# Kernel optimization log

Hardware: AMD Instinct MI355X
Metric: run time of the kernel (lower is better)

## Reference

```python
import jax, jax.numpy as jnp
import numpy as np

B, T, WN = 256, 200, 200        # batch, char_num, word_num
H, CD, WD = 512, 30, 128        # hidden_dim, char_dim, word_dim
V, K = 128, 12                  # vocab, tag_size
START, STOP = 10, 11
HH = H // 2


def lstm_dir(x_tm, m_tm, Wih, Whh, b, reverse):
    # x_tm: [T,B,I], m_tm: [T,B,1] validity mask. Packed-sequence semantics:
    # state only updates on valid steps, padded outputs are zero. reverse=True
    # replicates the backward direction of a packed bidirectional LSTM.
    z = jnp.zeros((x_tm.shape[1], Whh.shape[1]), x_tm.dtype)
    def cell(carry, inp):
        h, c = carry
        xt, mt = inp
        g = xt @ Wih.T + h @ Whh.T + b              # [B,4H], gates i,f,g,o
        i, f, gc, o = jnp.split(g, 4, axis=-1)
        cn = jax.nn.sigmoid(f) * c + jax.nn.sigmoid(i) * jnp.tanh(gc)
        hn = jax.nn.sigmoid(o) * jnp.tanh(cn)
        return (jnp.where(mt, hn, h), jnp.where(mt, cn, c)), jnp.where(mt, hn, 0.0)
    _, ys = jax.lax.scan(cell, (z, z), (x_tm, m_tm), reverse=reverse)
    return ys


def bilstm(x, lens, Wih_f, Whh_f, b_f, Wih_b, Whh_b, b_b):
    Tn = x.shape[1]
    m = jnp.arange(Tn)[None, :] < lens[:, None]     # [B,T]
    x_tm = jnp.swapaxes(x, 0, 1)
    m_tm = m.T[:, :, None]
    hf = lstm_dir(x_tm, m_tm, Wih_f, Whh_f, b_f, False)
    hb = lstm_dir(x_tm, m_tm, Wih_b, Whh_b, b_b, True)
    return jnp.swapaxes(jnp.concatenate([hf, hb], -1), 0, 1)  # [B,T,H]


def encode(characters, words, len_char, len_word,
           char_emb, char_Wih_f, char_Whh_f, char_b_f, char_Wih_b, char_Whh_b, char_b_b,
           char_lin_W, char_lin_b,
           word_Wih_f, word_Whh_f, word_b_f, word_Wih_b, word_Whh_b, word_b_b,
           word_lin_W, word_lin_b, lin1_W, lin1_b, lin2_W, lin2_b, tag_W, tag_b):
    sp = jax.nn.softplus
    char_vec = char_emb[characters]                                   # [B,T,CD]
    char_h = bilstm(char_vec, len_char, char_Wih_f, char_Whh_f, char_b_f,
                    char_Wih_b, char_Whh_b, char_b_b)                 # [B,T,H]
    char_map = sp(char_h @ char_lin_W.T + char_lin_b)                 # [B,T,H]
    word_h = bilstm(words, len_word, word_Wih_f, word_Whh_f, word_b_f,
                    word_Wih_b, word_Whh_b, word_b_b)                 # [B,WN,H]
    word_map = sp(word_h @ word_lin_W.T + word_lin_b)                 # [B,WN,T]
    word_map = word_map.reshape(word_map.shape[0], T, -1)             # view, NOT transpose
    x = jnp.concatenate([char_map, word_map], axis=2)                 # [B,T,712]
    x = sp(x @ lin1_W.T + lin1_b)
    x = sp(x @ lin2_W.T + lin2_b)
    return sp(x @ tag_W.T + tag_b)                                    # [B,T,K]


def crf_nll(logits, tags, lens, trans):
    Bn, Tn, Kn = logits.shape
    mask = jnp.arange(Tn)[None, :] < lens[:, None]                    # [B,T]
    # --- real path score (transitions indexed [from, to], START prepended) ---
    prev = jnp.concatenate([jnp.full((Bn, 1), START, tags.dtype), tags[:, :-1]], axis=1)
    emit = jnp.take_along_axis(logits, tags[..., None], axis=-1)[..., 0]
    step = jnp.where(mask, emit + trans[prev, tags], 0.0)
    last_tag = jnp.take_along_axis(tags, (lens - 1)[:, None], axis=1)[:, 0]
    real = step.sum(axis=1) + trans[last_tag, STOP]
    # --- forward algorithm (alpha init 0, first step includes transitions, as in source) ---
    def fwd(alpha, inp):
        lt, m = inp                                                   # [B,K], [B]
        sc = alpha[:, :, None] + lt[:, None, :] + trans[None]         # [B,prev,next]
        an = jax.nn.logsumexp(sc, axis=1)
        return jnp.where(m[:, None], an, alpha), None
    alpha0 = jnp.zeros((Bn, Kn), logits.dtype)
    alpha, _ = jax.lax.scan(fwd, alpha0, (jnp.swapaxes(logits, 0, 1), mask.T))
    total = jax.nn.logsumexp(alpha + trans[:, STOP][None, :], axis=1)
    return (jnp.sum(total) - jnp.sum(real)).reshape(1)


def setup_inputs() -> dict:
    key = jax.random.key(0)
    ks = jax.random.split(key, 32)
    rn = lambda k, s: jax.random.normal(k, s, jnp.float32) * 0.1
    inp = {
        "characters": jax.random.randint(ks[0], (B, T), 0, V),
        "words": jax.random.normal(ks[1], (B, WN, WD), jnp.float32),
        "tags": jax.random.randint(ks[2], (B, T), 0, K - 2),
        "len_char": jax.random.randint(ks[3], (B,), 50, T + 1),
        "len_word": jax.random.randint(ks[4], (B,), 50, WN + 1),
        "char_emb": rn(ks[5], (V, CD)),
        "char_Wih_f": rn(ks[6], (4 * HH, CD)), "char_Whh_f": rn(ks[7], (4 * HH, HH)), "char_b_f": rn(ks[8], (4 * HH,)),
        "char_Wih_b": rn(ks[9], (4 * HH, CD)), "char_Whh_b": rn(ks[10], (4 * HH, HH)), "char_b_b": rn(ks[11], (4 * HH,)),
        "char_lin_W": rn(ks[12], (H, H)), "char_lin_b": rn(ks[13], (H,)),
        "word_Wih_f": rn(ks[14], (4 * HH, WD)), "word_Whh_f": rn(ks[15], (4 * HH, HH)), "word_b_f": rn(ks[16], (4 * HH,)),
        "word_Wih_b": rn(ks[17], (4 * HH, WD)), "word_Whh_b": rn(ks[18], (4 * HH, HH)), "word_b_b": rn(ks[19], (4 * HH,)),
        "word_lin_W": rn(ks[20], (T, H)), "word_lin_b": rn(ks[21], (T,)),
        "lin1_W": rn(ks[22], (512, H + WN)), "lin1_b": rn(ks[23], (512,)),
        "lin2_W": rn(ks[24], (256, 512)), "lin2_b": rn(ks[25], (256,)),
        "tag_W": rn(ks[26], (K, 256)), "tag_b": rn(ks[27], (K,)),
    }
    trans = jax.random.normal(ks[28], (K, K), jnp.float32)
    trans = trans.at[START, :].set(-10000.0).at[:, STOP].set(-10000.0)
    inp["transitions"] = trans
    return inp


def reference(characters, words, tags, len_char, len_word,
              char_emb, char_Wih_f, char_Whh_f, char_b_f, char_Wih_b, char_Whh_b, char_b_b,
              char_lin_W, char_lin_b,
              word_Wih_f, word_Whh_f, word_b_f, word_Wih_b, word_Whh_b, word_b_b,
              word_lin_W, word_lin_b, lin1_W, lin1_b, lin2_W, lin2_b, tag_W, tag_b, transitions):
    logits = encode(characters, words, len_char, len_word,
                    char_emb, char_Wih_f, char_Whh_f, char_b_f, char_Wih_b, char_Whh_b, char_b_b,
                    char_lin_W, char_lin_b,
                    word_Wih_f, word_Whh_f, word_b_f, word_Wih_b, word_Whh_b, word_b_b,
                    word_lin_W, word_lin_b, lin1_W, lin1_b, lin2_W, lin2_b, tag_W, tag_b)
    return crf_nll(logits, tags, len_char, transitions)
```

## Files before the change

### kernel.cpp

```cpp
#include <hip/hip_runtime.h>
#include <cstdint>

typedef __attribute__((ext_vector_type(8))) short short8;
typedef __attribute__((ext_vector_type(4))) float f32x4;
typedef __attribute__((ext_vector_type(2))) float f32x2;
typedef __attribute__((ext_vector_type(4))) int i32x4;
typedef unsigned short us16;
typedef unsigned char u8;

#define DEV __device__ __forceinline__

DEV u8 f2fp8(float f){
  int p = __builtin_amdgcn_cvt_pk_fp8_f32(f, f, 0, false);
  return (u8)(p & 0xFF);
}
template<int SEL> DEV float fp8tof(int dw){
#if __has_builtin(__builtin_amdgcn_cvt_f32_fp8)
  return __builtin_amdgcn_cvt_f32_fp8(dw, SEL);
#else
  int b = (dw >> (8*SEL)) & 255;
  int e = (b>>3)&15, m = b&7;
  float v;
  if (e){ union{unsigned u; float f;} x; x.u = (unsigned)(((e+120)<<23) | (m<<20)); v = x.f; }
  else v = (float)m * 0.001953125f;
  return (b & 128) ? -v : v;
#endif
}
DEV f32x4 dq8x4(int dw){
#if __has_builtin(__builtin_amdgcn_cvt_pk_f32_fp8)
  f32x2 lo = __builtin_amdgcn_cvt_pk_f32_fp8(dw, false);
  f32x2 hi = __builtin_amdgcn_cvt_pk_f32_fp8(dw, true);
  return (f32x4){lo.x, lo.y, hi.x, hi.y};
#else
  return (f32x4){fp8tof<0>(dw), fp8tof<1>(dw), fp8tof<2>(dw), fp8tof<3>(dw)};
#endif
}
DEV float fsig(float x){
  float e = __builtin_amdgcn_exp2f(-1.4426950408889634f * x);
  return __builtin_amdgcn_rcpf(1.0f + e);
}
DEV float ftanh(float x){
  float e = __builtin_amdgcn_exp2f(-2.8853900817779268f * x);
  return fmaf(2.0f, __builtin_amdgcn_rcpf(1.0f + e), -1.0f);
}
DEV float fsoftplus(float x){
  float ax = fabsf(x);
  float e = __builtin_amdgcn_exp2f(-1.4426950408889634f * ax);
  float l = 0.69314718055994531f * __builtin_amdgcn_logf(1.0f + e);
  return fmaxf(x, 0.0f) + l;
}
DEV f32x4 mfma16f8(long a, long b, f32x4 c){
  return __builtin_amdgcn_mfma_f32_16x16x32_fp8_fp8(a, b, c, 0, 0, 0);
}
DEV unsigned pk4fp8(float a, float b, float c, float d){
  unsigned lo = (unsigned)__builtin_amdgcn_cvt_pk_fp8_f32(a, b, 0, false) & 0xFFFFu;
  unsigned hi = (unsigned)__builtin_amdgcn_cvt_pk_fp8_f32(c, d, 0, false) & 0xFFFFu;
  return lo | (hi << 16);
}

DEV void lds_barrier(){
  asm volatile("s_waitcnt lgkmcnt(0)" ::: "memory");
  __builtin_amdgcn_s_barrier();
  asm volatile("" ::: "memory");
}



DEV void swz_lstm16_one(int tid, const float* __restrict__ W, u8* __restrict__ dst){
  int e = tid & 511, chunk = tid >> 9;
  int L = e >> 3, j = e & 7;
  int kc = chunk & 7, gt = (chunk >> 3) & 3, w = chunk >> 5;
  int g = gt * 256 + w * 16 + (L & 15);
  int k = kc * 32 + (L >> 4) * 8 + j;
  dst[tid] = f2fp8(W[g * 256 + k]);
}

DEV void ctab_one(int vd, int gcol, const float* __restrict__ emb,
                  const float* __restrict__ Wih, const float* __restrict__ bb,
                  u8* __restrict__ ctab){
  int v = vd & 127, dir = vd >> 7;
  float val[4];
  #pragma unroll
  for (int gt = 0; gt < 4; ++gt){
    int g = gt * 256 + gcol;
    float s = bb[g];
    for (int k = 0; k < 30; ++k) s += emb[v * 30 + k] * Wih[g * 30 + k];
    val[gt] = s;
  }
  unsigned pk = pk4fp8(val[0], val[1], val[2], val[3]);
  *(unsigned*)&ctab[((dir * 128 + v) * 256 + gcol) * 4] = pk;
}

DEV void swz_gin_one(int tid, const float* __restrict__ W, u8* __restrict__ dst){
  int e = tid & 511, chunk = tid >> 9;
  int L = e >> 3, j = e & 7;
  int kc = chunk & 3, ntile = chunk >> 2;
  int g = ntile * 16 + (L & 15);
  int k = kc * 32 + (L >> 4) * 8 + j;
  dst[tid] = f2fp8(W[g * 128 + k]);
}

DEV void swz_ffB_one(int tid, const float* W, int N, int Kd, int KCs, u8* dst){
  int e = tid & 511, chunk = tid >> 9;
  int L = e >> 3, j = e & 7;
  int kc = chunk % KCs; int nt = chunk / KCs;
  int g = nt * 16 + (L & 15);
  int k = kc * 32 + (L >> 4) * 8 + j;
  float v = (g < N && k < Kd) ? W[g * Kd + k] : 0.0f;
  dst[tid] = f2fp8(v);
}

DEV void swz_ffA_one(int tid, const float* W, int Kd, int KCs, u8* dst){
  int e = tid & 511, chunk = tid >> 9;
  int L = e >> 3, j = e & 7;
  int kc = chunk % KCs; int mt = chunk / KCs;
  int m = mt * 16 + (L & 15);
  int k = kc * 32 + (L >> 4) * 8 + j;
  float v = (k < Kd) ? W[m * Kd + k] : 0.0f;
  dst[tid] = f2fp8(v);
}

__global__ __launch_bounds__(256) void k_pre(
    const float* __restrict__ words, u8* __restrict__ words_f8,
    const float* __restrict__ WhhA, u8* dA, const float* __restrict__ WhhB, u8* dB,
    const float* __restrict__ WhhC, u8* dC, const float* __restrict__ WhhD, u8* dD,
    const float* __restrict__ emb,
    const float* __restrict__ cWihF, const float* __restrict__ cbF,
    const float* __restrict__ cWihB, const float* __restrict__ cbB,
    u8* __restrict__ ctab,
    const float* __restrict__ gWf, const float* __restrict__ gWb,
    u8* __restrict__ dgf, u8* __restrict__ dgb,
    const float* __restrict__ W1, u8* d1, const float* __restrict__ W2, u8* d2,
    const float* __restrict__ W5, u8* d5,
    const float* __restrict__ W3, u8* d3, const float* __restrict__ W4, u8* d4)
{
  const int b = blockIdx.x, tid = threadIdx.x;
  if (b < 6400){
    int i = b * 256 + tid;
    f32x4 v = ((const f32x4*)words)[i];
    ((unsigned*)words_f8)[i] = pk4fp8(v.x, v.y, v.z, v.w);
  } else if (b < 10496){
    int bb = b - 6400;
    if (bb < 1024)       swz_lstm16_one(bb * 256 + tid, WhhA, dA);
    else if (bb < 2048)  swz_lstm16_one((bb - 1024) * 256 + tid, WhhB, dB);
    else if (bb < 3072)  swz_lstm16_one((bb - 2048) * 256 + tid, WhhC, dC);
    else                 swz_lstm16_one((bb - 3072) * 256 + tid, WhhD, dD);
  } else if (b < 10752){
    int vd = b - 10496;
    ctab_one(vd, tid, emb, (vd >> 7) ? cWihB : cWihF, (vd >> 7) ? cbB : cbF, ctab);
  } else if (b < 11776){
    int bb = b - 10752;
    if (bb < 512) swz_gin_one(bb * 256 + tid, gWf, dgf);
    else          swz_gin_one((bb - 512) * 256 + tid, gWb, dgb);
  } else if (b < 13328){
    int bb = b - 11776;
    if (bb < 1024)      swz_ffB_one(bb * 256 + tid, W1, 512, 512, 16, d1);
    else if (bb < 1536) swz_ffB_one((bb - 1024) * 256 + tid, W2, 200, 512, 16, d2);
    else                swz_ffB_one((bb - 1536) * 256 + tid, W5, 12, 256, 8, d5);
  } else {
    int bb = b - 13328;
    if (bb < 1536) swz_ffA_one(bb * 256 + tid, W3, 712, 24, d3);
    else           swz_ffA_one((bb - 1536) * 256 + tid, W4, 512, 16, d4);
  }
}

__global__ __launch_bounds__(512) void k_gin(
    const u8* __restrict__ words_f8, const u8* __restrict__ wswg_f,
    const u8* __restrict__ wswg_b, const float* __restrict__ bias_f,
    const float* __restrict__ bias_b, u8* __restrict__ gin)
{
  const int blk = blockIdx.x;
  const int d = blk / 800, rem = blk - d * 800;
  const int slice = rem / 50, tq = rem - slice * 50;
  const u8* Wsw = d ? wswg_b : wswg_f;
  const float* bias = d ? bias_b : bias_f;
  __shared__ u8 xs[16 * 136];
  __shared__ u8 sbuf[4 * 4096];
  const int tid = threadIdx.x;
  const int wv = tid >> 6, L = tid & 63;
  const int lrow = L & 15, lq = L >> 4;
  const long* WswV = (const long*)Wsw;

  long wr[8][4];
  #pragma unroll
  for (int nt = 0; nt < 8; ++nt)
    #pragma unroll
    for (int kc = 0; kc < 4; ++kc)
      wr[nt][kc] = WswV[((wv * 8 + nt) * 4 + kc) * 64 + L];
  float bv[8];
  #pragma unroll
  for (int nt = 0; nt < 8; ++nt) bv[nt] = bias[wv * 128 + nt * 16 + lrow];

  for (int i = 0; i < 4; ++i){
    const int t = tq * 4 + i;
    if (tid < 256){
      int r = tid >> 4, c8 = (tid & 15) * 8;
      *(long*)&xs[r * 136 + c8] =
        *(const long*)&words_f8[((long)(slice * 16 + r) * 200 + t) * 128 + c8];
    }
    __syncthreads();
    f32x4 acc[8];
    #pragma unroll
    for (int nt = 0; nt < 8; ++nt) acc[nt] = (f32x4){bv[nt], bv[nt], bv[nt], bv[nt]};
    #pragma unroll
    for (int kc = 0; kc < 4; ++kc){
      long af = *(const long*)&xs[lrow * 136 + kc * 32 + lq * 8];
      #pragma unroll
      for (int nt = 0; nt < 8; ++nt)
        acc[nt] = mfma16f8(af, wr[nt][kc], acc[nt]);
    }
    #pragma unroll
    for (int nt = 0; nt < 8; ++nt){
      int c = wv * 128 + nt * 16 + lrow;
      int gt = c >> 8, hcol = c & 255;
      int base = (hcol >> 4) * 256 + (hcol & 15) * 4 + gt;
      #pragma unroll
      for (int r = 0; r < 4; ++r)
        sbuf[lq * 4096 + base + r * 64] = f2fp8(acc[nt][r]);
    }
    __syncthreads();
    #pragma unroll
    for (int q = 0; q < 4; ++q){
      long ob = ((long)((d * 64 + slice * 4 + q) * 200 + t)) * 4096 + tid * 8;
      *(long*)&gin[ob] = *(const long*)&sbuf[q * 4096 + tid * 8];
    }
    __syncthreads();
  }
}

template<bool CHARV>
DEV void lstm16_body(u8* abuf, u8* cidxs,
                     const u8* __restrict__ gsrc,
                     const int* __restrict__ chars,
                     const u8* __restrict__ Wsw,
                     const int* __restrict__ lens,
                     u8* __restrict__ hout,
                     int b0, int hcol0, bool rev, long ginBase)
{
  const int tid = threadIdx.x;
  const int w = tid >> 6, L = tid & 63;
  const int lrow = L & 15, lq = L >> 4;
  const int gcol = w * 16 + lrow;
  const long* WswV = (const long*)Wsw;

  long wr[4][8];
  #pragma unroll
  for (int gt = 0; gt < 4; ++gt)
    #pragma unroll
    for (int kc = 0; kc < 8; ++kc)
      wr[gt][kc] = WswV[(((w * 4 + gt) * 8) + kc) * 64 + L];

  const int mylen = lens[b0 + lq];
  const long hbase = (long)(b0 + lq) * 200 * 512 + hcol0 + gcol;

  float cst = 0.0f;
  u8 hst = 0, houtv = 0;

  for (int e = tid; e < 1120; e += 1024) ((long*)abuf)[e] = 0;

  if constexpr (CHARV){
    if (tid < 800) cidxs[tid] = (u8)chars[(b0 + tid / 200) * 200 + tid % 200];
  }
  __syncthreads();

  const int t0 = rev ? 199 : 0;
  unsigned gw;
  if constexpr (!CHARV)
    gw = *(const unsigned*)(gsrc + (ginBase + t0) * 4096 + tid * 4);
  else
    gw = *(const unsigned*)&gsrc[((int)cidxs[lq * 200 + t0] * 256 + gcol) * 4];

  for (int tau = 0; tau < 200; ++tau){
    const int t = rev ? (199 - tau) : tau;
    u8* cur = abuf + (tau & 1) * 4480;
    u8* nxt = abuf + ((tau & 1) ^ 1) * 4480;

    f32x4 q = dq8x4((int)gw);
    f32x4 acc[4];
    #pragma unroll
    for (int gt = 0; gt < 4; ++gt)
      acc[gt] = (f32x4){q[gt], q[gt], q[gt], q[gt]};

    {
      const int tn = (tau < 199) ? (rev ? t - 1 : t + 1) : t;
      if constexpr (!CHARV)
        gw = *(const unsigned*)(gsrc + (ginBase + tn) * 4096 + tid * 4);
      else
        gw = *(const unsigned*)&gsrc[((int)cidxs[lq * 200 + tn] * 256 + gcol) * 4];
    }

    #pragma unroll
    for (int kc = 0; kc < 8; ++kc){
      long af = *(const long*)&cur[lrow * 280 + kc * 32 + lq * 8];
      #pragma unroll
      for (int gt = 0; gt < 4; ++gt)
        acc[gt] = mfma16f8(af, wr[gt][kc], acc[gt]);
    }

    const bool mk = t < mylen;
    float gi = acc[0][0], gf = acc[1][0];
    float gg = acc[2][0], go = acc[3][0];
    float cn = fsig(gf) * cst + fsig(gi) * ftanh(gg);
    if (mk) cst = cn;
    float hn = fsig(go) * ftanh(cn);
    u8 p8 = f2fp8(hn);
    if (mk) hst = p8;
    houtv = mk ? p8 : (u8)0;
    nxt[(lq * 4) * 280 + gcol] = hst;
    hout[hbase + (long)t * 512] = houtv;

    lds_barrier();
  }
}

__global__ __launch_bounds__(1024) void k_lstm(
    const int* __restrict__ characters, const u8* __restrict__ gin,
    const u8* __restrict__ ctab,
    const u8* __restrict__ wsw_cf, const u8* __restrict__ wsw_cb,
    const u8* __restrict__ wsw_wf, const u8* __restrict__ wsw_wb,
    const int* __restrict__ len_char, const int* __restrict__ len_word,
    u8* __restrict__ h_char, u8* __restrict__ h_word)
{
  const int dir    = blockIdx.x >> 6;
  const int slice4 = blockIdx.x & 63;
  const int b0 = slice4 * 4;
  __shared__ __align__(16) u8 abuf[2 * 16 * 280];
  __shared__ u8 cidxs[4 * 200];

  if (dir == 0)
    lstm16_body<true>(abuf, cidxs, ctab, characters, wsw_cf,
                      len_char, h_char, b0, 0, false, 0);
  else if (dir == 1)
    lstm16_body<true>(abuf, cidxs, ctab + 131072, characters, wsw_cb,
                      len_char, h_char, b0, 256, true, 0);
  else if (dir == 2)
    lstm16_body<false>(abuf, cidxs, gin, nullptr, wsw_wf,
                       len_word, h_word, b0, 0, false, (long)slice4 * 200);
  else
    lstm16_body<false>(abuf, cidxs, gin, nullptr, wsw_wb,
                       len_word, h_word, b0, 256, true, (long)(64 + slice4) * 200);
}

DEV void g12_body(const u8* __restrict__ A, const u8* __restrict__ Wsw,
                  const float* __restrict__ bias, int N,
                  u8* __restrict__ outp, int ocol0, int m0base, int ntbase, u8* lds)
{
  const int tid = threadIdx.x;
  const int w = tid >> 6, L = tid & 63;
  const int lrow = L & 15, lq = L >> 4;
  const long* WswV = (const long*)Wsw;
  f32x4 acc[8][2] = {};
  const int srow = tid >> 1, scol = (tid & 1) * 32;

  i32x4 v0 = *(const i32x4*)&A[(long)(m0base + srow) * 512 + scol];
  i32x4 v1 = *(const i32x4*)&A[(long)(m0base + srow) * 512 + scol + 16];

  for (int kc2 = 0; kc2 < 8; ++kc2){
    *(long*)&lds[srow * 72 + scol]      = ((const long*)&v0)[0];
    *(long*)&lds[srow * 72 + scol + 8]  = ((const long*)&v0)[1];
    *(long*)&lds[srow * 72 + scol + 16] = ((const long*)&v1)[0];
    *(long*)&lds[srow * 72 + scol + 24] = ((const long*)&v1)[1];
    lds_barrier();
    if (kc2 < 7){
      const long ab = (long)(m0base + srow) * 512 + (kc2 + 1) * 64 + scol;
      v0 = *(const i32x4*)&A[ab];
      v1 = *(const i32x4*)&A[ab + 16];
    }
    long af[2][2];
    #pragma unroll
    for (int m0 = 0; m0 < 2; ++m0)
      #pragma unroll
      for (int kk = 0; kk < 2; ++kk)
        af[m0][kk] = *(const long*)&lds[(w * 32 + m0 * 16 + lrow) * 72 + kk * 32 + lq * 8];
    #pragma unroll
    for (int kk = 0; kk < 2; ++kk)
      #pragma unroll
      for (int nt = 0; nt < 8; ++nt){
        long bf = WswV[((ntbase + nt) * 16 + kc2 * 2 + kk) * 64 + L];
        acc[nt][0] = mfma16f8(af[0][kk], bf, acc[nt][0]);
        acc[nt][1] = mfma16f8(af[1][kk], bf, acc[nt][1]);
      }
    lds_barrier();
  }
  #pragma unroll
  for (int nt = 0; nt < 8; ++nt){
    const int col = (ntbase + nt) * 16 + lrow;
    const bool valid = col < N;
    const float bvv = valid ? bias[col] : 0.0f;
    #pragma unroll
    for (int m0 = 0; m0 < 2; ++m0){
      #pragma unroll
      for (int r = 0; r < 4; ++r){
        float v = fsoftplus(acc[nt][m0][r] + bvv);
        const long row = m0base + w * 32 + m0 * 16 + lq * 4 + r;
        outp[row * 768 + ocol0 + col] = valid ? f2fp8(v) : (u8)0;
      }
    }
  }
}

__global__ __launch_bounds__(256) void k_g12(
    const u8* __restrict__ hc, const u8* __restrict__ hw,
    const u8* __restrict__ w1, const u8* __restrict__ w2,
    const float* __restrict__ b1, const float* __restrict__ b2,
    u8* __restrict__ xcat)
{
  __shared__ __align__(16) u8 lds[128 * 72];
  const int y = blockIdx.y;
  if (y < 4)
    g12_body(hc, w1, b1, 512, xcat,   0, blockIdx.x * 128, y * 8, lds);
  else
    g12_body(hw, w2, b2, 200, xcat, 512, blockIdx.x * 128, (y - 4) * 8, lds);
}

__global__ __launch_bounds__(256, 2) void k_tail(
    const u8* __restrict__ xcat, const u8* __restrict__ w3A,
    const u8* __restrict__ w4A, const u8* __restrict__ w5B,
    const float* __restrict__ b3, const float* __restrict__ b4,
    const float* __restrict__ b5, float* __restrict__ logits)
{
  __shared__ __align__(16) u8 sA[64 * 72];
  __shared__ __align__(16) u8 x1s[64 * 520];
  __shared__ __align__(16) u8 x2s[64 * 264];
  const int tid = threadIdx.x;
  const int w = tid >> 6, L = tid & 63;
  const int lrow = L & 15, lq = L >> 4;
  const int m0 = blockIdx.x * 64;
  const long* W3 = (const long*)w3A;
  const long* W4 = (const long*)w4A;
  const long* W5 = (const long*)w5B;

  f32x4 acc[8][4];
  #pragma unroll
  for (int mt = 0; mt < 8; ++mt)
    #pragma unroll
    for (int nt = 0; nt < 4; ++nt) acc[mt][nt] = (f32x4){0,0,0,0};
  const int srow = tid >> 2, sc = (tid & 3) * 16;

  i32x4 v = *(const i32x4*)&xcat[(long)(m0 + srow) * 768 + sc];
  for (int kc2 = 0; kc2 < 12; ++kc2){
    *(long*)&sA[srow * 72 + sc]     = ((const long*)&v)[0];
    *(long*)&sA[srow * 72 + sc + 8] = ((const long*)&v)[1];
    lds_barrier();
    if (kc2 < 11)
      v = *(const i32x4*)&xcat[(long)(m0 + srow) * 768 + (kc2 + 1) * 64 + sc];
    #pragma unroll
    for (int kk = 0; kk < 2; ++kk){
      long bf[4];
      #pragma unroll
      for (int nt = 0; nt < 4; ++nt)
        bf[nt] = *(const long*)&sA[(nt * 16 + lrow) * 72 + kk * 32 + lq * 8];
      #pragma unroll
      for (int mt = 0; mt < 8; ++mt){
        long af = W3[((w * 8 + mt) * 24 + kc2 * 2 + kk) * 64 + L];
        #pragma unroll
        for (int nt = 0; nt < 4; ++nt)
          acc[mt][nt] = mfma16f8(af, bf[nt], acc[mt][nt]);
      }
    }
    lds_barrier();
  }
  #pragma unroll
  for (int mt = 0; mt < 8; ++mt){
    const int ch0 = (w * 8 + mt) * 16 + lq * 4;
    f32x4 bb = *(const f32x4*)&b3[ch0];
    #pragma unroll
    for (int nt = 0; nt < 4; ++nt){
      const int bat = nt * 16 + lrow;
      unsigned pk = pk4fp8(fsoftplus(acc[mt][nt][0] + bb[0]),
                           fsoftplus(acc[mt][nt][1] + bb[1]),
                           fsoftplus(acc[mt][nt][2] + bb[2]),
                           fsoftplus(acc[mt][nt][3] + bb[3]));
      *(unsigned*)&x1s[bat * 520 + ch0] = pk;
    }
  }
  lds_barrier();

  f32x4 a2[4][4];
  #pragma unroll
  for (int mt = 0; mt < 4; ++mt)
    #pragma unroll
    for (int nt = 0; nt < 4; ++nt) a2[mt][nt] = (f32x4){0,0,0,0};
  for (int kc = 0; kc < 16; ++kc){
    long bf[4];
    #pragma unroll
    for (int nt = 0; nt < 4; ++nt)
      bf[nt] = *(const long*)&x1s[(nt * 16 + lrow) * 520 + kc * 32 + lq * 8];
    #pragma unroll
    for (int mt = 0; mt < 4; ++mt){
      long af = W4[((w * 4 + mt) * 16 + kc) * 64 + L];
      #pragma unroll
      for (int nt = 0; nt < 4; ++nt)
        a2[mt][nt] = mfma16f8(af, bf[nt], a2[mt][nt]);
    }
  }
  #pragma unroll
  for (int mt = 0; mt < 4; ++mt){
    const int ch0 = (w * 4 + mt) * 16 + lq * 4;
    f32x4 bb = *(const f32x4*)&b4[ch0];
    #pragma unroll
    for (int nt = 0; nt < 4; ++nt){
      const int bat = nt * 16 + lrow;
      unsigned pk = pk4fp8(fsoftplus(a2[mt][nt][0] + bb[0]),
                           fsoftplus(a2[mt][nt][1] + bb[1]),
                           fsoftplus(a2[mt][nt][2] + bb[2]),
                           fsoftplus(a2[mt][nt][3] + bb[3]));
      *(unsigned*)&x2s[bat * 264 + ch0] = pk;
    }
  }
  lds_barrier();

  f32x4 a3 = (f32x4){0,0,0,0};
  #pragma unroll
  for (int kc = 0; kc < 8; ++kc){
    long af = *(const long*)&x2s[(w * 16 + lrow) * 264 + kc * 32 + lq * 8];
    long bf = W5[kc * 64 + L];
    a3 = mfma16f8(af, bf, a3);
  }
  if (lrow < 12){
    float bb = b5[lrow];
    #pragma unroll
    for (int r = 0; r < 4; ++r)
      logits[(long)(m0 + w * 16 + lq * 4 + r) * 12 + lrow] = fsoftplus(a3[r] + bb);
  }
}

__global__ void k_crf(const float* __restrict__ logits, const int* __restrict__ tags,
                      const int* __restrict__ lens, const float* __restrict__ trans,
                      float* __restrict__ nll)
{
  const int b = blockIdx.x;
  const int lane = threadIdx.x;
  __shared__ float sl[2400];
  __shared__ float alpha[12];
  __shared__ float tmp[12];
  for (int e = lane; e < 2400; e += 64) sl[e] = logits[(long)b * 2400 + e];
  float tcol[12];
  if (lane < 12){
    #pragma unroll
    for (int i = 0; i < 12; ++i) tcol[i] = trans[i * 12 + lane];
    alpha[lane] = 0.0f;
  }
  const int len = lens[b];
  __syncthreads();
  for (int t = 0; t < len; ++t){
    float an = 0.0f;
    if (lane < 12){
      float mx = -3.0e38f;
      #pragma unroll
      for (int i = 0; i < 12; ++i) mx = fmaxf(mx, alpha[i] + tcol[i]);
      float ss = 0.0f;
      #pragma unroll
      for (int i = 0; i < 12; ++i)
        ss += __builtin_amdgcn_exp2f(1.4426950408889634f * (alpha[i] + tcol[i] - mx));
      an = sl[t * 12 + lane] + mx + 0.69314718055994531f * __builtin_amdgcn_logf(ss);
    }
    __syncthreads();
    if (lane < 12) alpha[lane] = an;
    __syncthreads();
  }
  if (lane < 12) tmp[lane] = alpha[lane] + trans[lane * 12 + 11];
  __syncthreads();
  float rs = 0.0f;
  for (int t = lane; t < len; t += 64){
    int tg = tags[b * 200 + t];
    int pv = (t == 0) ? 10 : tags[b * 200 + t - 1];
    rs += sl[t * 12 + tg] + trans[pv * 12 + tg];
  }
  #pragma unroll
  for (int off = 32; off > 0; off >>= 1) rs += __shfl_down(rs, off, 64);
  if (lane == 0){
    float mx = -3.0e38f;
    for (int i = 0; i < 12; ++i) mx = fmaxf(mx, tmp[i]);
    float ss = 0.0f;
    for (int i = 0; i < 12; ++i)
      ss += __builtin_amdgcn_exp2f(1.4426950408889634f * (tmp[i] - mx));
    float total = mx + 0.69314718055994531f * __builtin_amdgcn_logf(ss);
    rs += trans[tags[b * 200 + len - 1] * 12 + 11];
    nll[b] = total - rs;
  }
}

__global__ void k_sum(const float* __restrict__ nll, float* __restrict__ out){
  __shared__ float red[256];
  int t = threadIdx.x;
  red[t] = nll[t];
  __syncthreads();
  for (int s = 128; s > 0; s >>= 1){
    if (t < s) red[t] += red[t + s];
    __syncthreads();
  }
  if (t == 0) out[0] = red[0];
}

extern "C" void kernel_launch(void* const* d_in, const int* in_sizes, int n_in,
                              void* d_out, int out_size, void* d_ws, size_t ws_size,
                              hipStream_t stream)
{
  (void)in_sizes; (void)n_in; (void)out_size; (void)ws_size;
  const int*   characters = (const int*)  d_in[0];
  const float* words      = (const float*)d_in[1];
  const int*   tags       = (const int*)  d_in[2];
  const int*   len_char   = (const int*)  d_in[3];
  const int*   len_word   = (const int*)  d_in[4];
  const float* char_emb   = (const float*)d_in[5];
  const float* char_Wih_f = (const float*)d_in[6];
  const float* char_Whh_f = (const float*)d_in[7];
  const float* char_b_f   = (const float*)d_in[8];
  const float* char_Wih_b = (const float*)d_in[9];
  const float* char_Whh_b = (const float*)d_in[10];
  const float* char_b_b   = (const float*)d_in[11];
  const float* char_lin_W = (const float*)d_in[12];
  const float* char_lin_b = (const float*)d_in[13];
  const float* word_Wih_f = (const float*)d_in[14];
  const float* word_Whh_f = (const float*)d_in[15];
  const float* word_b_f   = (const float*)d_in[16];
  const float* word_Wih_b = (const float*)d_in[17];
  const float* word_Whh_b = (const float*)d_in[18];
  const float* word_b_b   = (const float*)d_in[19];
  const float* word_lin_W = (const float*)d_in[20];
  const float* word_lin_b = (const float*)d_in[21];
  const float* lin1_W     = (const float*)d_in[22];
  const float* lin1_b     = (const float*)d_in[23];
  const float* lin2_W     = (const float*)d_in[24];
  const float* lin2_b     = (const float*)d_in[25];
  const float* tag_W      = (const float*)d_in[26];
  const float* tag_b      = (const float*)d_in[27];
  const float* trans      = (const float*)d_in[28];

  char* ws = (char*)d_ws;
  size_t off = 0;
  auto take = [&](size_t bytes) -> char* {
    char* p = ws + off;
    off = (off + bytes + 511) & ~(size_t)511;
    return p;
  };
  u8*   words_f8 = (u8*)take((size_t)256*200*128);
  u8*   wsw_cf   = (u8*)take((size_t)262144);
  u8*   wsw_cb   = (u8*)take((size_t)262144);
  u8*   wsw_wf   = (u8*)take((size_t)262144);
  u8*   wsw_wb   = (u8*)take((size_t)262144);
  u8*   ctab     = (u8*)take((size_t)262144);
  u8*   wswgin_f = (u8*)take((size_t)64*4*512);
  u8*   wswgin_b = (u8*)take((size_t)64*4*512);
  u8*   wswg1    = (u8*)take((size_t)32*16*512);
  u8*   wswg2    = (u8*)take((size_t)16*16*512);
  u8*   wswg3    = (u8*)take((size_t)32*24*512);
  u8*   wswg4    = (u8*)take((size_t)16*16*512);
  u8*   wswg5    = (u8*)take((size_t)1*8*512);
  float* logits  = (float*)take((size_t)51200*12*4);
  float* nll     = (float*)take((size_t)256*4);
  u8*   h_char   = (u8*)take((size_t)51200*512);
  u8*   h_word   = (u8*)take((size_t)51200*512);
  u8*   gin      = (u8*)take((size_t)105*1024*1024);
  u8*   x_cat    = gin;

  k_pre<<<15376, 256, 0, stream>>>(
      words, words_f8,
      char_Whh_f, wsw_cf, char_Whh_b, wsw_cb, word_Whh_f, wsw_wf, word_Whh_b, wsw_wb,
      char_emb, char_Wih_f, char_b_f, char_Wih_b, char_b_b, ctab,
      word_Wih_f, word_Wih_b, wswgin_f, wswgin_b,
      char_lin_W, wswg1, word_lin_W, wswg2, tag_W, wswg5,
      lin1_W, wswg3, lin2_W, wswg4);

  k_gin<<<1600, 512, 0, stream>>>(words_f8, wswgin_f, wswgin_b, word_b_f, word_b_b, gin);

  k_lstm<<<256, 1024, 0, stream>>>(characters, gin, ctab,
                                   wsw_cf, wsw_cb, wsw_wf, wsw_wb,
                                   len_char, len_word, h_char, h_word);

  k_g12<<<dim3(400, 6), 256, 0, stream>>>(h_char, h_word, wswg1, wswg2,
                                          char_lin_b, word_lin_b, x_cat);
  k_tail<<<800, 256, 0, stream>>>(x_cat, wswg3, wswg4, wswg5,
                                  lin1_b, lin2_b, tag_b, logits);

  k_crf<<<256, 64, 0, stream>>>(logits, tags, len_char, trans, nll);
  k_sum<<<1, 256, 0, stream>>>(nll, (float*)d_out);
}
```

Before: 654.0 us.

## Fuse words fp8 conversion into gin GEMM, stage full A tiles, shuffle-based CRF

Removes the words-to-fp8 pass from k_pre and converts fp32 words to fp8 on the fly inside k_gin, dropping a global round trip. k_g12 and k_tail now load the whole K extent of A into LDS once, removing the per-chunk barriers, at the cost of much larger LDS use and lower occupancy (k_tail also loses its min-blocks launch bound). The CRF forward recursion keeps alpha in registers and uses wave shuffles instead of LDS plus two barriers per step.

```diff
diff --git a/kernel.cpp b/kernel.cpp
--- a/kernel.cpp
+++ b/kernel.cpp
@@ -121,7 +121,6 @@
 }
 
 __global__ __launch_bounds__(256) void k_pre(
-    const float* __restrict__ words, u8* __restrict__ words_f8,
     const float* __restrict__ WhhA, u8* dA, const float* __restrict__ WhhB, u8* dB,
     const float* __restrict__ WhhC, u8* dC, const float* __restrict__ WhhD, u8* dD,
     const float* __restrict__ emb,
@@ -135,37 +134,32 @@
     const float* __restrict__ W3, u8* d3, const float* __restrict__ W4, u8* d4)
 {
   const int b = blockIdx.x, tid = threadIdx.x;
-  if (b < 6400){
-    int i = b * 256 + tid;
-    f32x4 v = ((const f32x4*)words)[i];
-    ((unsigned*)words_f8)[i] = pk4fp8(v.x, v.y, v.z, v.w);
-  } else if (b < 10496){
-    int bb = b - 6400;
-    if (bb < 1024)       swz_lstm16_one(bb * 256 + tid, WhhA, dA);
-    else if (bb < 2048)  swz_lstm16_one((bb - 1024) * 256 + tid, WhhB, dB);
-    else if (bb < 3072)  swz_lstm16_one((bb - 2048) * 256 + tid, WhhC, dC);
-    else                 swz_lstm16_one((bb - 3072) * 256 + tid, WhhD, dD);
-  } else if (b < 10752){
-    int vd = b - 10496;
+  if (b < 4096){
+    if (b < 1024)       swz_lstm16_one(b * 256 + tid, WhhA, dA);
+    else if (b < 2048)  swz_lstm16_one((b - 1024) * 256 + tid, WhhB, dB);
+    else if (b < 3072)  swz_lstm16_one((b - 2048) * 256 + tid, WhhC, dC);
+    else                swz_lstm16_one((b - 3072) * 256 + tid, WhhD, dD);
+  } else if (b < 4352){
+    int vd = b - 4096;
     ctab_one(vd, tid, emb, (vd >> 7) ? cWihB : cWihF, (vd >> 7) ? cbB : cbF, ctab);
-  } else if (b < 11776){
-    int bb = b - 10752;
+  } else if (b < 5376){
+    int bb = b - 4352;
     if (bb < 512) swz_gin_one(bb * 256 + tid, gWf, dgf);
     else          swz_gin_one((bb - 512) * 256 + tid, gWb, dgb);
-  } else if (b < 13328){
-    int bb = b - 11776;
+  } else if (b < 6928){
+    int bb = b - 5376;
     if (bb < 1024)      swz_ffB_one(bb * 256 + tid, W1, 512, 512, 16, d1);
     else if (bb < 1536) swz_ffB_one((bb - 1024) * 256 + tid, W2, 200, 512, 16, d2);
     else                swz_ffB_one((bb - 1536) * 256 + tid, W5, 12, 256, 8, d5);
   } else {
-    int bb = b - 13328;
+    int bb = b - 6928;
     if (bb < 1536) swz_ffA_one(bb * 256 + tid, W3, 712, 24, d3);
     else           swz_ffA_one((bb - 1536) * 256 + tid, W4, 512, 16, d4);
   }
 }
 
 __global__ __launch_bounds__(512) void k_gin(
-    const u8* __restrict__ words_f8, const u8* __restrict__ wswg_f,
+    const float* __restrict__ words, const u8* __restrict__ wswg_f,
     const u8* __restrict__ wswg_b, const float* __restrict__ bias_f,
     const float* __restrict__ bias_b, u8* __restrict__ gin)
 {
@@ -193,10 +187,10 @@
 
   for (int i = 0; i < 4; ++i){
     const int t = tq * 4 + i;
-    if (tid < 256){
-      int r = tid >> 4, c8 = (tid & 15) * 8;
-      *(long*)&xs[r * 136 + c8] =
-        *(const long*)&words_f8[((long)(slice * 16 + r) * 200 + t) * 128 + c8];
+    {
+      int r = tid >> 5, c4 = (tid & 31) * 4;
+      f32x4 v = *(const f32x4*)&words[((long)(slice * 16 + r) * 200 + t) * 128 + c4];
+      *(unsigned*)&xs[r * 136 + c4] = pk4fp8(v.x, v.y, v.z, v.w);
     }
     __syncthreads();
     f32x4 acc[8];
@@ -349,38 +343,28 @@
   const int w = tid >> 6, L = tid & 63;
   const int lrow = L & 15, lq = L >> 4;
   const long* WswV = (const long*)Wsw;
+
+  {
+    const int row = tid >> 1, half = (tid & 1) * 256;
+    #pragma unroll
+    for (int q = 0; q < 16; ++q)
+      *(i32x4*)&lds[row * 520 + half + q * 16] =
+        *(const i32x4*)&A[(long)(m0base + row) * 512 + half + q * 16];
+  }
+  lds_barrier();
+
   f32x4 acc[8][2] = {};
-  const int srow = tid >> 1, scol = (tid & 1) * 32;
-
-  i32x4 v0 = *(const i32x4*)&A[(long)(m0base + srow) * 512 + scol];
-  i32x4 v1 = *(const i32x4*)&A[(long)(m0base + srow) * 512 + scol + 16];
-
-  for (int kc2 = 0; kc2 < 8; ++kc2){
-    *(long*)&lds[srow * 72 + scol]      = ((const long*)&v0)[0];
-    *(long*)&lds[srow * 72 + scol + 8]  = ((const long*)&v0)[1];
-    *(long*)&lds[srow * 72 + scol + 16] = ((const long*)&v1)[0];
-    *(long*)&lds[srow * 72 + scol + 24] = ((const long*)&v1)[1];
-    lds_barrier();
-    if (kc2 < 7){
-      const long ab = (long)(m0base + srow) * 512 + (kc2 + 1) * 64 + scol;
-      v0 = *(const i32x4*)&A[ab];
-      v1 = *(const i32x4*)&A[ab + 16];
-    }
-    long af[2][2];
+  for (int kc = 0; kc < 16; ++kc){
+    long af[2];
     #pragma unroll
     for (int m0 = 0; m0 < 2; ++m0)
-      #pragma unroll
-      for (int kk = 0; kk < 2; ++kk)
-        af[m0][kk] = *(const long*)&lds[(w * 32 + m0 * 16 + lrow) * 72 + kk * 32 + lq * 8];
-    #pragma unroll
-    for (int kk = 0; kk < 2; ++kk)
-      #pragma unroll
-      for (int nt = 0; nt < 8; ++nt){
-        long bf = WswV[((ntbase + nt) * 16 + kc2 * 2 + kk) * 64 + L];
-        acc[nt][0] = mfma16f8(af[0][kk], bf, acc[nt][0]);
-        acc[nt][1] = mfma16f8(af[1][kk], bf, acc[nt][1]);
-      }
-    lds_barrier();
+      af[m0] = *(const long*)&lds[(w * 32 + m0 * 16 + lrow) * 520 + kc * 32 + lq * 8];
+    #pragma unroll
+    for (int nt = 0; nt < 8; ++nt){
+      long bf = WswV[((ntbase + nt) * 16 + kc) * 64 + L];
+      acc[nt][0] = mfma16f8(af[0], bf, acc[nt][0]);
+      acc[nt][1] = mfma16f8(af[1], bf, acc[nt][1]);
+    }
   }
   #pragma unroll
   for (int nt = 0; nt < 8; ++nt){
@@ -405,7 +389,7 @@
     const float* __restrict__ b1, const float* __restrict__ b2,
     u8* __restrict__ xcat)
 {
-  __shared__ __align__(16) u8 lds[128 * 72];
+  __shared__ __align__(16) u8 lds[128 * 520];
   const int y = blockIdx.y;
   if (y < 4)
     g12_body(hc, w1, b1, 512, xcat,   0, blockIdx.x * 128, y * 8, lds);
@@ -413,13 +397,13 @@
     g12_body(hw, w2, b2, 200, xcat, 512, blockIdx.x * 128, (y - 4) * 8, lds);
 }
 
-__global__ __launch_bounds__(256, 2) void k_tail(
+__global__ __launch_bounds__(256) void k_tail(
     const u8* __restrict__ xcat, const u8* __restrict__ w3A,
     const u8* __restrict__ w4A, const u8* __restrict__ w5B,
     const float* __restrict__ b3, const float* __restrict__ b4,
     const float* __restrict__ b5, float* __restrict__ logits)
 {
-  __shared__ __align__(16) u8 sA[64 * 72];
+  __shared__ __align__(16) u8 sA[64 * 776];
   __shared__ __align__(16) u8 x1s[64 * 520];
   __shared__ __align__(16) u8 x2s[64 * 264];
   const int tid = threadIdx.x;
@@ -430,26 +414,28 @@
   const long* W4 = (const long*)w4A;
   const long* W5 = (const long*)w5B;
 
+  {
+    const int row = tid >> 2, seg = (tid & 3) * 192;
+    #pragma unroll
+    for (int q = 0; q < 12; ++q)
+      *(i32x4*)&sA[row * 776 + seg + q * 16] =
+        *(const i32x4*)&xcat[(long)(m0 + row) * 768 + seg + q * 16];
+  }
+  lds_barrier();
+
   f32x4 acc[8][4];
   #pragma unroll
   for (int mt = 0; mt < 8; ++mt)
     #pragma unroll
     for (int nt = 0; nt < 4; ++nt) acc[mt][nt] = (f32x4){0,0,0,0};
-  const int srow = tid >> 2, sc = (tid & 3) * 16;
-
-  i32x4 v = *(const i32x4*)&xcat[(long)(m0 + srow) * 768 + sc];
+
   for (int kc2 = 0; kc2 < 12; ++kc2){
-    *(long*)&sA[srow * 72 + sc]     = ((const long*)&v)[0];
-    *(long*)&sA[srow * 72 + sc + 8] = ((const long*)&v)[1];
-    lds_barrier();
-    if (kc2 < 11)
-      v = *(const i32x4*)&xcat[(long)(m0 + srow) * 768 + (kc2 + 1) * 64 + sc];
     #pragma unroll
     for (int kk = 0; kk < 2; ++kk){
       long bf[4];
       #pragma unroll
       for (int nt = 0; nt < 4; ++nt)
-        bf[nt] = *(const long*)&sA[(nt * 16 + lrow) * 72 + kk * 32 + lq * 8];
+        bf[nt] = *(const long*)&sA[(nt * 16 + lrow) * 776 + kc2 * 64 + kk * 32 + lq * 8];
       #pragma unroll
       for (int mt = 0; mt < 8; ++mt){
         long af = W3[((w * 8 + mt) * 24 + kc2 * 2 + kk) * 64 + L];
@@ -458,7 +444,6 @@
           acc[mt][nt] = mfma16f8(af, bf[nt], acc[mt][nt]);
       }
     }
-    lds_barrier();
   }
   #pragma unroll
   for (int mt = 0; mt < 8; ++mt){
@@ -532,35 +517,39 @@
   const int b = blockIdx.x;
   const int lane = threadIdx.x;
   __shared__ float sl[2400];
-  __shared__ float alpha[12];
-  __shared__ float tmp[12];
   for (int e = lane; e < 2400; e += 64) sl[e] = logits[(long)b * 2400 + e];
+  const int lj = (lane < 12) ? lane : 0;
   float tcol[12];
-  if (lane < 12){
-    #pragma unroll
-    for (int i = 0; i < 12; ++i) tcol[i] = trans[i * 12 + lane];
-    alpha[lane] = 0.0f;
-  }
+  #pragma unroll
+  for (int i = 0; i < 12; ++i) tcol[i] = trans[i * 12 + lj];
   const int len = lens[b];
+  float alpha = 0.0f;
   __syncthreads();
+
   for (int t = 0; t < len; ++t){
-    float an = 0.0f;
-    if (lane < 12){
-      float mx = -3.0e38f;
-      #pragma unroll
-      for (int i = 0; i < 12; ++i) mx = fmaxf(mx, alpha[i] + tcol[i]);
-      float ss = 0.0f;
-      #pragma unroll
-      for (int i = 0; i < 12; ++i)
-        ss += __builtin_amdgcn_exp2f(1.4426950408889634f * (alpha[i] + tcol[i] - mx));
-      an = sl[t * 12 + lane] + mx + 0.69314718055994531f * __builtin_amdgcn_logf(ss);
-    }
-    __syncthreads();
-    if (lane < 12) alpha[lane] = an;
-    __syncthreads();
-  }
-  if (lane < 12) tmp[lane] = alpha[lane] + trans[lane * 12 + 11];
-  __syncthreads();
+    float av[12];
+    #pragma unroll
+    for (int i = 0; i < 12; ++i)
+      av[i] = __shfl(alpha, i, 64) + tcol[i];
+    float mx = av[0];
+    #pragma unroll
+    for (int i = 1; i < 12; ++i) mx = fmaxf(mx, av[i]);
+    float ss = 0.0f;
+    #pragma unroll
+    for (int i = 0; i < 12; ++i)
+      ss += __builtin_amdgcn_exp2f(1.4426950408889634f * (av[i] - mx));
+    alpha = sl[t * 12 + lj] + mx + 0.69314718055994531f * __builtin_amdgcn_logf(ss);
+  }
+
+  float tv = alpha + trans[lj * 12 + 11];
+  float tmax = tv;
+  #pragma unroll
+  for (int i = 0; i < 12; ++i) tmax = fmaxf(tmax, __shfl(tv, i, 64));
+  float tss = 0.0f;
+  #pragma unroll
+  for (int i = 0; i < 12; ++i)
+    tss += __builtin_amdgcn_exp2f(1.4426950408889634f * (__shfl(tv, i, 64) - tmax));
+
   float rs = 0.0f;
   for (int t = lane; t < len; t += 64){
     int tg = tags[b * 200 + t];
@@ -570,12 +559,7 @@
   #pragma unroll
   for (int off = 32; off > 0; off >>= 1) rs += __shfl_down(rs, off, 64);
   if (lane == 0){
-    float mx = -3.0e38f;
-    for (int i = 0; i < 12; ++i) mx = fmaxf(mx, tmp[i]);
-    float ss = 0.0f;
-    for (int i = 0; i < 12; ++i)
-      ss += __builtin_amdgcn_exp2f(1.4426950408889634f * (tmp[i] - mx));
-    float total = mx + 0.69314718055994531f * __builtin_amdgcn_logf(ss);
+    float total = tmax + 0.69314718055994531f * __builtin_amdgcn_logf(tss);
     rs += trans[tags[b * 200 + len - 1] * 12 + 11];
     nll[b] = total - rs;
   }
@@ -635,7 +619,6 @@
     off = (off + bytes + 511) & ~(size_t)511;
     return p;
   };
-  u8*   words_f8 = (u8*)take((size_t)256*200*128);
   u8*   wsw_cf   = (u8*)take((size_t)262144);
   u8*   wsw_cb   = (u8*)take((size_t)262144);
   u8*   wsw_wf   = (u8*)take((size_t)262144);
@@ -655,15 +638,14 @@
   u8*   gin      = (u8*)take((size_t)105*1024*1024);
   u8*   x_cat    = gin;
 
-  k_pre<<<15376, 256, 0, stream>>>(
-      words, words_f8,
+  k_pre<<<8976, 256, 0, stream>>>(
       char_Whh_f, wsw_cf, char_Whh_b, wsw_cb, word_Whh_f, wsw_wf, word_Whh_b, wsw_wb,
       char_emb, char_Wih_f, char_b_f, char_Wih_b, char_b_b, ctab,
       word_Wih_f, word_Wih_b, wswgin_f, wswgin_b,
       char_lin_W, wswg1, word_lin_W, wswg2, tag_W, wswg5,
       lin1_W, wswg3, lin2_W, wswg4);
 
-  k_gin<<<1600, 512, 0, stream>>>(words_f8, wswgin_f, wswgin_b, word_b_f, word_b_b, gin);
+  k_gin<<<1600, 512, 0, stream>>>(words, wswgin_f, wswgin_b, word_b_f, word_b_b, gin);
 
   k_lstm<<<256, 1024, 0, stream>>>(characters, gin, ctab,
                                    wsw_cf, wsw_cb, wsw_wf, wsw_wb,
```

Measured after the change: 677.6 us. 1.04x slower.
